# Kernel tuning notes

Measured on AMD Instinct MI355X. Metric: run time of the kernel, lower is better.

## Reference

```python
import jax, jax.numpy as jnp
import numpy as np

B, C, L = 4, 64, 4096
RED = 4          # reduction -> q/k channels = C // RED = 16
N_HASHES = 4
HASH_BUCKETS = min(L // 4, 32)  # = 32, matches torch code
EPS = 1e-5


def _conv1x1(x, W, b):
    # x: [B, Cin, L], W: [Cout, Cin], b: [Cout]
    return jnp.einsum('bcl,oc->bol', x, W) + b[None, :, None]


def setup_inputs() -> dict:
    key = jax.random.key(0)
    ks = jax.random.split(key, 12)
    Cq = C // RED
    x = jax.random.normal(ks[0], (B, C, L), dtype=jnp.float32)
    hash_idx = jax.random.randint(ks[1], (B, N_HASHES, L), 0, HASH_BUCKETS, dtype=jnp.int32)
    sC = 1.0 / np.sqrt(C)
    Wq = jax.random.normal(ks[2], (Cq, C), dtype=jnp.float32) * sC
    bq = jax.random.normal(ks[3], (Cq,), dtype=jnp.float32) * 0.01
    Wk = jax.random.normal(ks[4], (Cq, C), dtype=jnp.float32) * sC
    bk = jax.random.normal(ks[5], (Cq,), dtype=jnp.float32) * 0.01
    Wv = jax.random.normal(ks[6], (C, C), dtype=jnp.float32) * sC
    bv = jax.random.normal(ks[7], (C,), dtype=jnp.float32) * 0.01
    Wo = jax.random.normal(ks[8], (C, C), dtype=jnp.float32) * sC
    bo = jax.random.normal(ks[9], (C,), dtype=jnp.float32) * 0.01
    gamma = jax.random.normal(ks[10], (1,), dtype=jnp.float32)  # nonzero so attn path matters
    bn_w = jnp.ones((C,), dtype=jnp.float32)
    bn_b = jnp.zeros((C,), dtype=jnp.float32)
    return dict(x=x, hash_idx=hash_idx, Wq=Wq, bq=bq, Wk=Wk, bk=bk,
                Wv=Wv, bv=bv, Wo=Wo, bo=bo, gamma=gamma, bn_w=bn_w, bn_b=bn_b)


def reference(x, hash_idx, Wq, bq, Wk, bk, Wv, bv, Wo, bo, gamma, bn_w, bn_b):
    # 1x1 conv projections
    q = _conv1x1(x, Wq, bq)   # [B, C/RED, L]
    k = _conv1x1(x, Wk, bk)   # [B, C/RED, L]
    v = _conv1x1(x, Wv, bv)   # [B, C, L]

    qT = q.transpose(0, 2, 1)  # [B, L, Cq]
    kT = k.transpose(0, 2, 1)
    vT = v.transpose(0, 2, 1)  # [B, L, C]

    # raw scores are hash-independent; only the bucket mask changes per hash
    scores = jnp.einsum('bic,bjc->bij', qT, kT)  # [B, L, L], no sqrt(d) scaling (matches torch)

    n_hashes = hash_idx.shape[1]
    acc = jnp.zeros_like(vT)
    for h in range(n_hashes):  # small fixed loop
        idx = hash_idx[:, h, :]                       # [B, L]
        mask = idx[:, :, None] == idx[:, None, :]     # same-bucket mask [B, L, L]
        s = jnp.where(mask, scores, -1e9)
        attn = jax.nn.softmax(s, axis=-1)             # within-bucket softmax (diag always valid)
        acc = acc + jnp.einsum('bij,bjc->bic', attn, vT)
    attn_out = (acc / n_hashes).transpose(0, 2, 1)    # [B, C, L], averaged over hashes

    out = _conv1x1(attn_out, Wo, bo)
    out = gamma * out + x                             # residual with learned scalar

    # BatchNorm1d, training mode: biased batch stats over (B, L) per channel
    mean = out.mean(axis=(0, 2), keepdims=True)
    var = out.var(axis=(0, 2), keepdims=True)
    out = (out - mean) * jax.lax.rsqrt(var + EPS)
    out = out * bn_w[None, :, None] + bn_b[None, :, None]
    return out
```

## Files before the change

### kernel.cpp

```cpp
#include <hip/hip_runtime.h>
#include <math.h>

#define Bn 4
#define Cn 64
#define Ln 4096
#define CQ 16
#define NH 4
#define NB 32
#define EPSV 1e-5f

#define MAXS 384
#define CH2 64
#define KSTR 20
#define VSTR 64

#define QSZ   (Bn*Ln*CQ)
#define VSZ   (Bn*Ln*Cn)
#define ACCSZ (Bn*Ln*Cn)
#define NBH   (Bn*NH)

#define OFF_K   QSZ
#define OFF_V   (2*QSZ)
#define OFF_ACC (2*QSZ + VSZ)

#define LOG2E 1.44269504088896f

__global__ __launch_bounds__(256) void proj_kernel(
        const float* __restrict__ x,
        const float* __restrict__ Wq, const float* __restrict__ bq,
        const float* __restrict__ Wk, const float* __restrict__ bk,
        const float* __restrict__ Wv, const float* __restrict__ bv,
        float* __restrict__ q, float* __restrict__ k, float* __restrict__ v) {
    __shared__ float sWt[Cn*32];
    __shared__ float sb[32];
    int tid = threadIdx.x;
    int third = blockIdx.x % 3;
    int pg    = blockIdx.x / 3;
    int rbase = third * 32;
    for (int idx = tid; idx < Cn*32; idx += 256) {
        int rr = idx & 31, c = idx >> 5;
        int r = rbase + rr;
        float w;
        if (r < 16)      w = Wq[r*Cn + c];
        else if (r < 32) w = Wk[(r-16)*Cn + c];
        else             w = Wv[(r-32)*Cn + c];
        sWt[c*32 + rr] = w;
    }
    if (tid < 32) {
        int r = rbase + tid;
        sb[tid] = (r < 16) ? bq[r] : (r < 32 ? bk[r-16] : bv[r-32]);
    }
    __syncthreads();
    int p = tid & 63, og = tid >> 6;
    int gp = pg * 64 + p;
    int b = gp >> 12, l = gp & (Ln - 1);
    const float* xp = &x[b*Cn*Ln + l];
    int rr0 = og * 8;
    float val[8];
    #pragma unroll
    for (int i = 0; i < 8; i++) val[i] = sb[rr0 + i];
    #pragma unroll
    for (int c0 = 0; c0 < Cn; c0 += 8) {
        float xv[8];
        #pragma unroll
        for (int i = 0; i < 8; i++) xv[i] = xp[(c0 + i)*Ln];
        #pragma unroll
        for (int i = 0; i < 8; i++) {
            const float* wrow = &sWt[(c0 + i)*32 + rr0];
            #pragma unroll
            for (int j = 0; j < 8; j++) val[j] = fmaf(wrow[j], xv[i], val[j]);
        }
    }
    int f = third*8 + og*2;
    float4 t0 = make_float4(val[0], val[1], val[2], val[3]);
    float4 t1 = make_float4(val[4], val[5], val[6], val[7]);
    float4* q4 = (float4*)&q[gp*CQ];
    float4* k4 = (float4*)&k[gp*CQ];
    float4* v4 = (float4*)&v[gp*Cn];
    if (f < 4)      { q4[f]   = t0; q4[f+1] = t1; }
    else if (f < 8) { k4[f-4] = t0; k4[f-3] = t1; }
    else            { v4[f-8] = t0; v4[f-7] = t1; }
}

template<int NS, int MODE>
__device__ __forceinline__ void attn_pass(
        int qbase, int S, int b, int h, int tid, int rem,
        const int* list, float* ks, float* vs,
        const float* __restrict__ q, const float* __restrict__ k,
        const float* __restrict__ v, float* __restrict__ acc) {
    int qd = tid >> 2, c4 = tid & 3;
    float4 qr[NS][4];
    float4 o[NS][4];
    float lsum[NS];
    int qi[NS], iqr[NS];
    #pragma unroll
    for (int s = 0; s < NS; s++) {
        qi[s] = qbase + 64*s + qd;
        iqr[s] = 0;
        lsum[s] = 0.f;
        #pragma unroll
        for (int i = 0; i < 4; i++) o[s][i] = make_float4(0.f,0.f,0.f,0.f);
        if (qi[s] < S) {
            iqr[s] = list[qi[s]];
            const float4* qp = (const float4*)&q[((size_t)b*Ln + iqr[s])*CQ];
            #pragma unroll
            for (int i = 0; i < 4; i++) {
                float4 t = qp[i];
                t.x*=LOG2E; t.y*=LOG2E; t.z*=LOG2E; t.w*=LOG2E;
                qr[s][i] = t;
            }
        } else {
            #pragma unroll
            for (int i = 0; i < 4; i++) qr[s][i] = make_float4(0.f,0.f,0.f,0.f);
        }
    }
    for (int cc = 0; cc < S; cc += CH2) {
        int nk = min(CH2, S - cc);
        __syncthreads();
        {
            int jj = tid >> 2, cf = tid & 3;
            if (jj < nk) {
                const float4* kp = (const float4*)&k[((size_t)b*Ln + list[cc+jj])*CQ];
                *(float4*)&ks[jj*KSTR + cf*4] = kp[cf];
            }
        }
        #pragma unroll
        for (int uu = 0; uu < 4; uu++) {
            int idx = uu*256 + tid;
            int jj = idx >> 4, cf = idx & 15;
            if (jj < nk) {
                const float4* vp = (const float4*)&v[((size_t)b*Ln + list[cc+jj])*Cn];
                *(float4*)&vs[jj*VSTR + cf*4] = vp[cf];
            }
        }
        __syncthreads();
        if (rem > 0) {
            for (int j = 0; j < nk; j++) {
                const float4* kr = (const float4*)&ks[j*KSTR];
                float4 k0 = kr[0], k1 = kr[1], k2 = kr[2], k3 = kr[3];
                const float4* vp4 = (const float4*)&vs[j*VSTR + c4*16];
                float4 v0 = vp4[0], v1 = vp4[1], v2 = vp4[2], v3 = vp4[3];
                #pragma unroll
                for (int s = 0; s < NS; s++) {
                    float s0 = qr[s][0].x*k0.x + qr[s][0].y*k0.y + qr[s][0].z*k0.z + qr[s][0].w*k0.w;
                    float s1 = qr[s][1].x*k1.x + qr[s][1].y*k1.y + qr[s][1].z*k1.z + qr[s][1].w*k1.w;
                    float s2 = qr[s][2].x*k2.x + qr[s][2].y*k2.y + qr[s][2].z*k2.z + qr[s][2].w*k2.w;
                    float s3 = qr[s][3].x*k3.x + qr[s][3].y*k3.y + qr[s][3].z*k3.z + qr[s][3].w*k3.w;
                    float pw = __builtin_amdgcn_exp2f((s0 + s1) + (s2 + s3));
                    lsum[s] += pw;
                    o[s][0].x = fmaf(pw, v0.x, o[s][0].x); o[s][0].y = fmaf(pw, v0.y, o[s][0].y);
                    o[s][0].z = fmaf(pw, v0.z, o[s][0].z); o[s][0].w = fmaf(pw, v0.w, o[s][0].w);
                    o[s][1].x = fmaf(pw, v1.x, o[s][1].x); o[s][1].y = fmaf(pw, v1.y, o[s][1].y);
                    o[s][1].z = fmaf(pw, v1.z, o[s][1].z); o[s][1].w = fmaf(pw, v1.w, o[s][1].w);
                    o[s][2].x = fmaf(pw, v2.x, o[s][2].x); o[s][2].y = fmaf(pw, v2.y, o[s][2].y);
                    o[s][2].z = fmaf(pw, v2.z, o[s][2].z); o[s][2].w = fmaf(pw, v2.w, o[s][2].w);
                    o[s][3].x = fmaf(pw, v3.x, o[s][3].x); o[s][3].y = fmaf(pw, v3.y, o[s][3].y);
                    o[s][3].z = fmaf(pw, v3.z, o[s][3].z); o[s][3].w = fmaf(pw, v3.w, o[s][3].w);
                }
            }
        }
    }
    #pragma unroll
    for (int s = 0; s < NS; s++) {
        if (qi[s] < S) {
            float inv = 1.f / lsum[s];
            #pragma unroll
            for (int i = 0; i < 4; i++) {
                o[s][i].x*=inv; o[s][i].y*=inv; o[s][i].z*=inv; o[s][i].w*=inv;
            }
            if (MODE == 1) {
                float4* ap = (float4*)&acc[((size_t)h*Bn*Ln + b*Ln + iqr[s])*Cn + c4*16];
                ap[0]=o[s][0]; ap[1]=o[s][1]; ap[2]=o[s][2]; ap[3]=o[s][3];
            } else {
                float* ap = &acc[((size_t)b*Ln + iqr[s])*Cn + c4*16];
                #pragma unroll
                for (int i = 0; i < 4; i++) {
                    atomicAdd(&ap[4*i+0], (&o[s][i].x)[0]);
                    atomicAdd(&ap[4*i+1], (&o[s][i].x)[1]);
                    atomicAdd(&ap[4*i+2], (&o[s][i].x)[2]);
                    atomicAdd(&ap[4*i+3], (&o[s][i].x)[3]);
                }
            }
        }
    }
}

template<int MODE>
__global__ __launch_bounds__(256, 2) void attn_kernel(
        const float* __restrict__ q, const float* __restrict__ k,
        const float* __restrict__ v, const int* __restrict__ hidx,
        float* __restrict__ acc) {
    __shared__ int list[MAXS];
    __shared__ float ks[CH2*KSTR];
    __shared__ float vs[CH2*VSTR];
    __shared__ int wtot[4];
    int blk = blockIdx.x;
    int u  = blk & (NB-1);
    int bh = blk >> 5;
    int b  = bh >> 2;
    int h  = bh & 3;
    int tid = threadIdx.x;

    const int4* hp4 = (const int4*)(&hidx[bh*Ln] + tid*16);
    int hv[16];
    #pragma unroll
    for (int t = 0; t < 4; t++) {
        int4 tmp = hp4[t];
        hv[t*4+0]=tmp.x; hv[t*4+1]=tmp.y; hv[t*4+2]=tmp.z; hv[t*4+3]=tmp.w;
    }
    int myCnt = 0;
    #pragma unroll
    for (int t = 0; t < 16; t++) myCnt += (hv[t] == u);
    int lane = tid & 63, wv = tid >> 6;
    int pre = myCnt;
    #pragma unroll
    for (int d = 1; d < 64; d <<= 1) {
        int t = __shfl_up(pre, d, 64);
        if (lane >= d) pre += t;
    }
    if (lane == 63) wtot[wv] = pre;
    __syncthreads();
    int base = 0;
    #pragma unroll
    for (int w = 0; w < 4; w++) base += (w < wv) ? wtot[w] : 0;
    int Sall = wtot[0] + wtot[1] + wtot[2] + wtot[3];
    int S = min(Sall, MAXS);
    int excl = base + pre - myCnt;
    #pragma unroll
    for (int t = 0; t < 16; t++) {
        if (hv[t] == u) {
            if (excl < MAXS) list[excl] = tid*16 + t;
            excl++;
        }
    }
    __syncthreads();

    int wq0 = (tid >> 6) << 4;
    for (int qbase = 0; qbase < S; qbase += 192) {
        int rem = S - qbase - wq0;
        if (rem > 128)     attn_pass<3,MODE>(qbase,S,b,h,tid,rem,list,ks,vs,q,k,v,acc);
        else if (rem > 64) attn_pass<2,MODE>(qbase,S,b,h,tid,rem,list,ks,vs,q,k,v,acc);
        else               attn_pass<1,MODE>(qbase,S,b,h,tid,rem,list,ks,vs,q,k,v,acc);
    }
}

template<int MODE>
__global__ __launch_bounds__(256) void outconv_kernel(
        const float* __restrict__ acc, const float* __restrict__ Wo,
        const float* __restrict__ bo, const float* __restrict__ gamma,
        const float* __restrict__ x, float* __restrict__ y) {
    __shared__ float sWt[Cn*Cn];
    __shared__ float sA[Cn*33];
    __shared__ float sb[Cn];
    int tid = threadIdx.x;
    int pg = blockIdx.x;
    for (int idx = tid; idx < Cn*Cn; idx += 256) {
        int o = idx & 63, c = idx >> 6;
        sWt[c*Cn + o] = Wo[o*Cn + c];
    }
    if (tid < Cn) sb[tid] = bo[tid];
    const float4* a4 = (const float4*)&acc[(size_t)pg*32*Cn];
    #pragma unroll
    for (int r = 0; r < 2; r++) {
        int idx = r*256 + tid;
        int p = idx >> 4, c0 = (idx & 15) * 4;
        float4 t = a4[idx];
        if (MODE == 1) {
            float4 t1 = a4[(size_t)ACCSZ/4   + idx];
            float4 t2 = a4[(size_t)ACCSZ/4*2 + idx];
            float4 t3 = a4[(size_t)ACCSZ/4*3 + idx];
            t.x += t1.x + t2.x + t3.x; t.y += t1.y + t2.y + t3.y;
            t.z += t1.z + t2.z + t3.z; t.w += t1.w + t2.w + t3.w;
        }
        sA[(c0+0)*33 + p] = t.x*0.25f;
        sA[(c0+1)*33 + p] = t.y*0.25f;
        sA[(c0+2)*33 + p] = t.z*0.25f;
        sA[(c0+3)*33 + p] = t.w*0.25f;
    }
    __syncthreads();
    float g = gamma[0];
    int p = tid & 31, og = tid >> 5;
    int gp = pg * 32 + p;
    int b = gp >> 12, l = gp & (Ln - 1);
    int o0 = og * 8;
    float val[8];
    #pragma unroll
    for (int i = 0; i < 8; i++) val[i] = sb[o0 + i];
    #pragma unroll
    for (int c = 0; c < Cn; c++) {
        float av = sA[c*33 + p];
        const float* wrow = &sWt[c*Cn + o0];
        #pragma unroll
        for (int i = 0; i < 8; i++) val[i] = fmaf(wrow[i], av, val[i]);
    }
    #pragma unroll
    for (int i = 0; i < 8; i++) {
        int o = o0 + i;
        float yv = fmaf(g, val[i], x[(b*Cn + o)*Ln + l]);
        y[(b*Cn + o)*Ln + l] = yv;
    }
}

__global__ __launch_bounds__(256) void stats_kernel(
        const float* __restrict__ y, float* __restrict__ ssumP, float* __restrict__ ssqP) {
    int c = blockIdx.x >> 2;
    int part = blockIdx.x & 3;
    int tid = threadIdx.x;
    const float4* yp = (const float4*)&y[(part*Cn + c)*Ln];
    float s = 0.f, s2 = 0.f;
    #pragma unroll
    for (int i = 0; i < 4; i++) {
        float4 t = yp[i*256 + tid];
        s  += t.x + t.y + t.z + t.w;
        s2 += t.x*t.x + t.y*t.y + t.z*t.z + t.w*t.w;
    }
    #pragma unroll
    for (int w = 1; w < 64; w <<= 1) {
        s  += __shfl_xor(s,  w, 64);
        s2 += __shfl_xor(s2, w, 64);
    }
    __shared__ float rs[4], rs2[4];
    int wv = tid >> 6;
    if ((tid & 63) == 0) { rs[wv] = s; rs2[wv] = s2; }
    __syncthreads();
    if (tid == 0) {
        ssumP[blockIdx.x] = rs[0]+rs[1]+rs[2]+rs[3];
        ssqP[blockIdx.x]  = rs2[0]+rs2[1]+rs2[2]+rs2[3];
    }
}

__global__ __launch_bounds__(256) void norm_kernel(
        const float* __restrict__ y,
        const float* __restrict__ ssumP, const float* __restrict__ ssqP,
        const float* __restrict__ bnw, const float* __restrict__ bnb,
        float* __restrict__ out) {
    int idx = blockIdx.x * 256 + threadIdx.x;
    int flat = idx * 4;
    int c = (flat / Ln) & 63;
    float s = 0.f, s2 = 0.f;
    #pragma unroll
    for (int hh = 0; hh < 4; hh++) { s += ssumP[c*4+hh]; s2 += ssqP[c*4+hh]; }
    const float n = (float)(Bn*Ln);
    float mu = s / n;
    float var = s2 / n - mu*mu;
    float is = rsqrtf(var + EPSV);
    float w = is * bnw[c];
    float bb = bnb[c] - mu * w;
    float4 t = ((const float4*)y)[idx];
    float4 r;
    r.x = t.x*w + bb; r.y = t.y*w + bb; r.z = t.z*w + bb; r.w = t.w*w + bb;
    ((float4*)out)[idx] = r;
}

extern "C" void kernel_launch(void* const* d_in, const int* in_sizes, int n_in,
                              void* d_out, int out_size, void* d_ws, size_t ws_size,
                              hipStream_t stream) {
    const float* x    = (const float*)d_in[0];
    const int*   hidx = (const int*)  d_in[1];
    const float* Wq   = (const float*)d_in[2];
    const float* bq   = (const float*)d_in[3];
    const float* Wk   = (const float*)d_in[4];
    const float* bk   = (const float*)d_in[5];
    const float* Wv   = (const float*)d_in[6];
    const float* bv   = (const float*)d_in[7];
    const float* Wo   = (const float*)d_in[8];
    const float* bo   = (const float*)d_in[9];
    const float* gam  = (const float*)d_in[10];
    const float* bnw  = (const float*)d_in[11];
    const float* bnb  = (const float*)d_in[12];
    float* out = (float*)d_out;

    float* ws  = (float*)d_ws;
    float* q   = ws;
    float* k   = ws + OFF_K;
    float* v   = ws + OFF_V;
    float* acc = ws + OFF_ACC;
    float* y   = ws;

    const size_t bigNeed = ((size_t)OFF_ACC + 4*(size_t)ACCSZ + 512) * sizeof(float);
    bool big = ws_size >= bigNeed;
    float* ssumP = acc + (big ? 4*(size_t)ACCSZ : (size_t)ACCSZ);
    float* ssqP  = ssumP + 256;

    proj_kernel<<<Bn*Ln/64*3, 256, 0, stream>>>(x, Wq, bq, Wk, bk, Wv, bv, q, k, v);
    if (big) {
        attn_kernel<1><<<NBH*NB, 256, 0, stream>>>(q, k, v, hidx, acc);
        outconv_kernel<1><<<Bn*Ln/32, 256, 0, stream>>>(acc, Wo, bo, gam, x, y);
    } else {
        hipMemsetAsync(acc, 0, (size_t)ACCSZ*sizeof(float), stream);
        attn_kernel<0><<<NBH*NB, 256, 0, stream>>>(q, k, v, hidx, acc);
        outconv_kernel<0><<<Bn*Ln/32, 256, 0, stream>>>(acc, Wo, bo, gam, x, y);
    }
    stats_kernel<<<Cn*4, 256, 0, stream>>>(y, ssumP, ssqP);
    norm_kernel<<<Bn*Cn*Ln/4/256, 256, 0, stream>>>(y, ssumP, ssqP, bnw, bnb, out);
}
```

Measured before the change: 169.8 us.

## Split attention queries across two blocks per bucket and quad-reduce scores via DPP

Each (batch, hash, bucket) is now processed by two blocks that take interleaved 64-query chunks, which doubles the grid to 1024 blocks for better CU fill. Each thread of a quad now holds only its quarter of the query vector and computes a partial dot product, and DPP swizzles sum the four partials. This cuts query registers, so launch bounds are raised to allow 4 blocks per CU. The cost is that every block rebuilds the bucket list and reloads all K/V for its bucket, doubling K/V traffic, and each score now needs two cross-lane DPP ops.

```diff
diff --git a/kernel.cpp b/kernel.cpp
--- a/kernel.cpp
+++ b/kernel.cpp
@@ -13,6 +13,9 @@
 #define CH2 64
 #define KSTR 20
 #define VSTR 64
+
+#define QSPLIT 2
+#define QSTRIDE (64*QSPLIT)
 
 #define QSZ   (Bn*Ln*CQ)
 #define VSZ   (Bn*Ln*Cn)
@@ -82,6 +85,12 @@
     else            { v4[f-8] = t0; v4[f-7] = t1; }
 }
 
+__device__ __forceinline__ float quad_reduce_sum(float d) {
+    d += __int_as_float(__builtin_amdgcn_mov_dpp(__float_as_int(d), 0xB1, 0xF, 0xF, true));
+    d += __int_as_float(__builtin_amdgcn_mov_dpp(__float_as_int(d), 0x4E, 0xF, 0xF, true));
+    return d;
+}
+
 template<int NS, int MODE>
 __device__ __forceinline__ void attn_pass(
         int qbase, int S, int b, int h, int tid, int rem,
@@ -89,13 +98,13 @@
         const float* __restrict__ q, const float* __restrict__ k,
         const float* __restrict__ v, float* __restrict__ acc) {
     int qd = tid >> 2, c4 = tid & 3;
-    float4 qr[NS][4];
+    float4 qr[NS];
     float4 o[NS][4];
     float lsum[NS];
     int qi[NS], iqr[NS];
     #pragma unroll
     for (int s = 0; s < NS; s++) {
-        qi[s] = qbase + 64*s + qd;
+        qi[s] = qbase + QSTRIDE*s + qd;
         iqr[s] = 0;
         lsum[s] = 0.f;
         #pragma unroll
@@ -103,15 +112,11 @@
         if (qi[s] < S) {
             iqr[s] = list[qi[s]];
             const float4* qp = (const float4*)&q[((size_t)b*Ln + iqr[s])*CQ];
-            #pragma unroll
-            for (int i = 0; i < 4; i++) {
-                float4 t = qp[i];
-                t.x*=LOG2E; t.y*=LOG2E; t.z*=LOG2E; t.w*=LOG2E;
-                qr[s][i] = t;
-            }
+            float4 t = qp[c4];
+            t.x*=LOG2E; t.y*=LOG2E; t.z*=LOG2E; t.w*=LOG2E;
+            qr[s] = t;
         } else {
-            #pragma unroll
-            for (int i = 0; i < 4; i++) qr[s][i] = make_float4(0.f,0.f,0.f,0.f);
+            qr[s] = make_float4(0.f,0.f,0.f,0.f);
         }
     }
     for (int cc = 0; cc < S; cc += CH2) {
@@ -136,17 +141,17 @@
         __syncthreads();
         if (rem > 0) {
             for (int j = 0; j < nk; j++) {
-                const float4* kr = (const float4*)&ks[j*KSTR];
-                float4 k0 = kr[0], k1 = kr[1], k2 = kr[2], k3 = kr[3];
+                float4 kq = *(const float4*)&ks[j*KSTR + c4*4];
                 const float4* vp4 = (const float4*)&vs[j*VSTR + c4*16];
                 float4 v0 = vp4[0], v1 = vp4[1], v2 = vp4[2], v3 = vp4[3];
                 #pragma unroll
                 for (int s = 0; s < NS; s++) {
-                    float s0 = qr[s][0].x*k0.x + qr[s][0].y*k0.y + qr[s][0].z*k0.z + qr[s][0].w*k0.w;
-                    float s1 = qr[s][1].x*k1.x + qr[s][1].y*k1.y + qr[s][1].z*k1.z + qr[s][1].w*k1.w;
-                    float s2 = qr[s][2].x*k2.x + qr[s][2].y*k2.y + qr[s][2].z*k2.z + qr[s][2].w*k2.w;
-                    float s3 = qr[s][3].x*k3.x + qr[s][3].y*k3.y + qr[s][3].z*k3.z + qr[s][3].w*k3.w;
-                    float pw = __builtin_amdgcn_exp2f((s0 + s1) + (s2 + s3));
+                    float d = qr[s].x*kq.x;
+                    d = fmaf(qr[s].y, kq.y, d);
+                    d = fmaf(qr[s].z, kq.z, d);
+                    d = fmaf(qr[s].w, kq.w, d);
+                    d = quad_reduce_sum(d);
+                    float pw = __builtin_amdgcn_exp2f(d);
                     lsum[s] += pw;
                     o[s][0].x = fmaf(pw, v0.x, o[s][0].x); o[s][0].y = fmaf(pw, v0.y, o[s][0].y);
                     o[s][0].z = fmaf(pw, v0.z, o[s][0].z); o[s][0].w = fmaf(pw, v0.w, o[s][0].w);
@@ -186,7 +191,7 @@
 }
 
 template<int MODE>
-__global__ __launch_bounds__(256, 2) void attn_kernel(
+__global__ __launch_bounds__(256, 4) void attn_kernel(
         const float* __restrict__ q, const float* __restrict__ k,
         const float* __restrict__ v, const int* __restrict__ hidx,
         float* __restrict__ acc) {
@@ -195,8 +200,9 @@
     __shared__ float vs[CH2*VSTR];
     __shared__ int wtot[4];
     int blk = blockIdx.x;
+    int qs = blk >> 9;
     int u  = blk & (NB-1);
-    int bh = blk >> 5;
+    int bh = (blk >> 5) & (NBH-1);
     int b  = bh >> 2;
     int h  = bh & 3;
     int tid = threadIdx.x;
@@ -236,11 +242,11 @@
     __syncthreads();
 
     int wq0 = (tid >> 6) << 4;
-    for (int qbase = 0; qbase < S; qbase += 192) {
+    for (int qbase = qs*64; qbase < S; qbase += 3*QSTRIDE) {
         int rem = S - qbase - wq0;
-        if (rem > 128)     attn_pass<3,MODE>(qbase,S,b,h,tid,rem,list,ks,vs,q,k,v,acc);
-        else if (rem > 64) attn_pass<2,MODE>(qbase,S,b,h,tid,rem,list,ks,vs,q,k,v,acc);
-        else               attn_pass<1,MODE>(qbase,S,b,h,tid,rem,list,ks,vs,q,k,v,acc);
+        if (rem > 2*QSTRIDE)      attn_pass<3,MODE>(qbase,S,b,h,tid,rem,list,ks,vs,q,k,v,acc);
+        else if (rem > QSTRIDE)   attn_pass<2,MODE>(qbase,S,b,h,tid,rem,list,ks,vs,q,k,v,acc);
+        else                      attn_pass<1,MODE>(qbase,S,b,h,tid,rem,list,ks,vs,q,k,v,acc);
     }
 }
 
@@ -384,11 +390,11 @@
 
     proj_kernel<<<Bn*Ln/64*3, 256, 0, stream>>>(x, Wq, bq, Wk, bk, Wv, bv, q, k, v);
     if (big) {
-        attn_kernel<1><<<NBH*NB, 256, 0, stream>>>(q, k, v, hidx, acc);
+        attn_kernel<1><<<NBH*NB*QSPLIT, 256, 0, stream>>>(q, k, v, hidx, acc);
         outconv_kernel<1><<<Bn*Ln/32, 256, 0, stream>>>(acc, Wo, bo, gam, x, y);
     } else {
         hipMemsetAsync(acc, 0, (size_t)ACCSZ*sizeof(float), stream);
-        attn_kernel<0><<<NBH*NB, 256, 0, stream>>>(q, k, v, hidx, acc);
+        attn_kernel<0><<<NBH*NB*QSPLIT, 256, 0, stream>>>(q, k, v, hidx, acc);
         outconv_kernel<0><<<Bn*Ln/32, 256, 0, stream>>>(acc, Wo, bo, gam, x, y);
     }
     stats_kernel<<<Cn*4, 256, 0, stream>>>(y, ssumP, ssqP);
```

Result: faster. 155.2 us (-8.6%).
